# Performance work log

Measured on AMD Instinct MI355X. Metric: run time of the kernel, lower is better.

The kernel has to match this reference:

```python
import jax, jax.numpy as jnp
from jax import lax
import numpy as np

N_MTF = 41

def _gaussian2d(N, std):
    t = np.arange(-(N - 1) / 2, (N + 1) / 2)
    t1, t2 = np.meshgrid(t, t)
    return np.exp(-0.5 * (t1 / std) ** 2) * np.exp(-0.5 * (t2 / std) ** 2)

def _kaiser2d(N, beta):
    t = np.arange(-(N - 1) / 2, (N + 1) / 2) / np.double(N - 1)
    t1, t2 = np.meshgrid(t, t)
    t12 = np.sqrt(t1 * t1 + t2 * t2)
    w1 = np.kaiser(N, beta)
    w = np.interp(t12, t, w1)
    w[t12 > t[-1]] = 0
    w[t12 < t[0]] = 0
    return w

def _fir_filter_wind(Hd, w):
    hd = np.rot90(np.fft.fftshift(np.rot90(Hd, 2)), 2)
    h = np.fft.fftshift(np.fft.ifft2(hd))
    h = np.rot90(h, 2)
    return h * w

def gen_mtf_kernels(ratio, nbands):
    GNyq = np.asarray([0.34, 0.32, 0.3, 0.22], dtype='float32')[:nbands]  # QB sensor
    h = np.zeros((nbands, N_MTF, N_MTF), dtype='float32')
    fcut = 1.0 / ratio
    for ii in range(nbands):
        alpha = np.sqrt(((N_MTF - 1) * (fcut / 2)) ** 2 / (-2 * np.log(GNyq[ii])))
        H = _gaussian2d(N_MTF, alpha)
        Hd = H / np.max(H)
        w = _kaiser2d(N_MTF, 0.5)
        h[ii] = np.real(_fir_filter_wind(Hd, w)).astype('float32')
    return h

def gen_interp23_kernel():
    cdf23 = 2.0 * np.array([0.5, 0.305334091185, 0.0, -0.072698593239, 0.0,
                            0.021809577942, 0.0, -0.005192756653, 0.0,
                            0.000807762146, 0.0, -6.0081482e-05])
    d = cdf23[::-1]
    return np.concatenate([d[:-1], cdf23]).astype('float32')  # 23 taps

_DN = ('NCHW', 'OIHW', 'NCHW')

def _sep_filter_circular(img, k):
    # img: (bs, c, H, W); k: (K,) separable kernel, circular padding per torch F.pad('circular')
    bs, c, H, W = img.shape
    P = (k.shape[0] - 1) // 2
    f = img.reshape(bs * c, 1, H, W)
    f = jnp.pad(f, ((0, 0), (0, 0), (0, 0), (P, P)), mode='wrap')
    f = lax.conv_general_dilated(f, k.reshape(1, 1, 1, -1), (1, 1), 'VALID', dimension_numbers=_DN)
    f = jnp.pad(f, ((0, 0), (0, 0), (P, P), (0, 0)), mode='wrap')
    f = lax.conv_general_dilated(f, k.reshape(1, 1, -1, 1), (1, 1), 'VALID', dimension_numbers=_DN)
    return f.reshape(bs, c, H, W)

def interp23tap(x, kernel, num_upsamples):
    cur = x
    for k in range(num_upsamples):
        bs, c, h, w = cur.shape
        up = jnp.zeros((bs, c, 2 * h, 2 * w), cur.dtype)
        if k == 0:
            up = up.at[..., 1::2, 1::2].set(cur)
        else:
            up = up.at[..., ::2, ::2].set(cur)
        cur = _sep_filter_circular(up, kernel)
    return cur

def setup_inputs() -> dict:
    key = jax.random.key(0)
    bs, nbands, H, W = 4, 4, 1024, 1024
    ratio = 4
    x = jax.random.normal(key, (bs, nbands, H, W), dtype=jnp.float32)
    mtf_kernels = jnp.asarray(gen_mtf_kernels(ratio, nbands))          # (nbands, 41, 41)
    interp_kernel = jnp.asarray(gen_interp23_kernel())                  # (23,)
    pan_weights = jnp.full((nbands,), 1.0 / nbands, dtype=jnp.float32)  # 'mean' pan weights
    return {"x": x, "mtf_kernels": mtf_kernels, "interp_kernel": interp_kernel,
            "pan_weights": pan_weights, "ratio": ratio}

def reference(x, mtf_kernels, interp_kernel, pan_weights, ratio):
    # Simulated PAN: spectral weighting of HR bands
    pan = jnp.einsum('bchw,c->bhw', x, pan_weights)[:, None]  # (bs,1,H,W)
    # MTF blur: depthwise 41x41 conv with replicate padding
    nbands = x.shape[1]
    pad = mtf_kernels.shape[-1] // 2
    xp = jnp.pad(x, ((0, 0), (0, 0), (pad, pad), (pad, pad)), mode='edge')
    blurred = lax.conv_general_dilated(xp, mtf_kernels[:, None], (1, 1), 'VALID',
                                       dimension_numbers=_DN, feature_group_count=nbands)
    # Downsample: avgpool with kernel=stride=ratio
    bs, c, H, W = blurred.shape
    lrms = blurred.reshape(bs, c, H // ratio, ratio, W // ratio, ratio).mean(axis=(3, 5))
    # Upsample back via 23-tap polynomial interpolation (ratio = 2**num_upsamples)
    num_ups = int(ratio).bit_length() - 1
    ms_up = interp23tap(lrms, interp_kernel, num_ups)
    return pan, lrms, ms_up
```

## Files before the change

kernel.cpp:

```cpp
#include <hip/hip_runtime.h>

#define LRMS_OFF 4194304
#define MS_OFF  5242880

__global__ __launch_bounds__(256) void build_keff_kernel(
    const float* __restrict__ mtf, float* __restrict__ keff) {
  int e = blockIdx.x * 256 + threadIdx.x;
  if (e >= 4 * 44 * 44) return;
  int c = e / 1936;
  int rem = e - c * 1936;
  int p = rem / 44;
  int q = rem - p * 44;
  float s = 0.f;
  for (int di = 0; di < 4; ++di) {
    int u = p - di;
    if (u < 0 || u > 40) continue;
    for (int dj = 0; dj < 4; ++dj) {
      int v = q - dj;
      if (v < 0 || v > 40) continue;
      s += mtf[(c * 41 + u) * 41 + v];
    }
  }
  keff[e] = s * 0.0625f;
}

__global__ void build_gcoef_kernel(const float* __restrict__ ik,
                                   float* __restrict__ G) {
  int tid = threadIdx.x;
  if (tid >= 68) return;
  int d = tid / 17, oi = tid % 17, o = oi - 8;
  float k2[12];
  #pragma unroll
  for (int t = 0; t < 12; ++t) k2[t] = ik[2 * t];
  float g = 0.f;
  if (d == 0) {
    int t = o + 6;
    if (t >= 0 && t < 12) g = k2[t];
  } else if (d == 2) {
    g = (o == 0) ? 1.f : 0.f;
  } else if (d == 1) {
    int t = 2 * (o + 3);
    if (t >= 0 && t <= 10) g += k2[t];
    for (int t1 = 1; t1 < 12; t1 += 2) {
      int r = o + 6 - (t1 - 5) / 2;
      if (r >= 0 && r < 12) g += k2[t1] * k2[r];
    }
  } else {
    int t = 2 * o + 5;
    if (t >= 1 && t <= 11) g += k2[t];
    for (int t0 = 0; t0 <= 10; t0 += 2) {
      int r = o + 8 - t0 / 2;
      if (r >= 0 && r < 12) g += k2[t0] * k2[r];
    }
  }
  G[d * 17 + oi] = g;
}

__global__ __launch_bounds__(256) void pan_kernel(
    const float* __restrict__ x, const float* __restrict__ w,
    float* __restrict__ pan) {
  int g = blockIdx.x * 256 + threadIdx.x;
  int b = g >> 18;
  int e = g & 262143;
  const float4* x4 = (const float4*)x;
  float w0 = w[0], w1 = w[1], w2 = w[2], w3 = w[3];
  float4 a0 = x4[(size_t)(b * 4 + 0) * 262144 + e];
  float4 a1 = x4[(size_t)(b * 4 + 1) * 262144 + e];
  float4 a2 = x4[(size_t)(b * 4 + 2) * 262144 + e];
  float4 a3 = x4[(size_t)(b * 4 + 3) * 262144 + e];
  float4 o;
  o.x = a0.x * w0 + a1.x * w1 + a2.x * w2 + a3.x * w3;
  o.y = a0.y * w0 + a1.y * w1 + a2.y * w2 + a3.y * w3;
  o.z = a0.z * w0 + a1.z * w1 + a2.z * w2 + a3.z * w3;
  o.w = a0.w * w0 + a1.w * w1 + a2.w * w2 + a3.w * w3;
  ((float4*)pan)[g] = o;
}

__global__ __launch_bounds__(256) void lrms_kernel(
    const float* __restrict__ x, const float* __restrict__ keff,
    float* __restrict__ lrms) {
  int img = blockIdx.y;
  int ch  = img & 3;
  int i0  = blockIdx.x * 4;
  int oc  = threadIdx.x;

  const float* ximg = x + (size_t)img * 1048576;
  const float* Kc   = keff + ch * 1936;

  float4 acc[4];
  #pragma unroll
  for (int r = 0; r < 4; ++r) acc[r] = make_float4(0.f, 0.f, 0.f, 0.f);

  int c4base = oc - 5;
  bool interior = (oc >= 5) && (oc <= 250);
  float4 va[11], vb[11];

  auto loadrow = [&](int tt, float4* v) {
    int gy = 4 * i0 - 20 + tt;
    gy = gy < 0 ? 0 : (gy > 1023 ? 1023 : gy);
    const float4* row4 = (const float4*)(ximg + (size_t)gy * 1024);
    if (interior) {
      #pragma unroll
      for (int a = 0; a < 11; ++a) v[a] = row4[c4base + a];
    } else {
      const float* rowf = (const float*)row4;
      #pragma unroll
      for (int a = 0; a < 11; ++a) {
        int c4 = c4base + a;
        if ((unsigned)c4 <= 255u) {
          v[a] = row4[c4];
        } else {
          float4 t;
          t.x = rowf[min(max(4 * c4 + 0, 0), 1023)];
          t.y = rowf[min(max(4 * c4 + 1, 0), 1023)];
          t.z = rowf[min(max(4 * c4 + 2, 0), 1023)];
          t.w = rowf[min(max(4 * c4 + 3, 0), 1023)];
          v[a] = t;
        }
      }
    }
  };

  auto compute = [&](int tt, const float4* v) {
    #pragma unroll
    for (int r = 0; r < 4; ++r) {
      int p = tt - 4 * r;
      if ((unsigned)p < 44u) {
        const float* Kr = Kc + __builtin_amdgcn_readfirstlane(p * 44);
        float4 s = acc[r];
        #pragma unroll
        for (int a = 0; a < 11; ++a) {
          s.x += v[a].x * Kr[4 * a + 0];
          s.y += v[a].y * Kr[4 * a + 1];
          s.z += v[a].z * Kr[4 * a + 2];
          s.w += v[a].w * Kr[4 * a + 3];
        }
        acc[r] = s;
      }
    }
  };

  loadrow(0, va);
  for (int it = 0; it < 28; ++it) {
    int tt = 2 * it;
    loadrow(tt + 1, vb);
    compute(tt, va);
    if (tt + 2 < 56) loadrow(tt + 2, va);
    compute(tt + 1, vb);
  }

  #pragma unroll
  for (int r = 0; r < 4; ++r) {
    float s = acc[r].x + acc[r].y + acc[r].z + acc[r].w;
    lrms[((size_t)img * 256 + i0 + r) * 256 + oc] = s;
  }
}

__global__ __launch_bounds__(256) void interp_kernel(
    const float* __restrict__ lrms, const float* __restrict__ G,
    float* __restrict__ ms) {
  __shared__ float lr[32][48];
  __shared__ float H[32][68];
  __shared__ float Gs[4][17];

  int img = blockIdx.z;
  int bx = blockIdx.x, by = blockIdx.y;
  int tid = threadIdx.x;

  if (tid < 68) Gs[tid / 17][tid % 17] = G[tid];

  const float* L = lrms + (size_t)img * 65536;
  int ybase = by * 16 - 8, xbase = bx * 16 - 8;
  for (int e = tid; e < 1024; e += 256) {
    int yy = e >> 5, xx = e & 31;
    lr[yy][xx] = L[((ybase + yy) & 255) * 256 + ((xbase + xx) & 255)];
  }
  __syncthreads();

  for (int u = tid; u < 512; u += 256) {
    int r = u >> 4, j = u & 15;
    float t[17];
    #pragma unroll
    for (int o = 0; o < 17; ++o) t[o] = lr[r][j + o];
    float h0 = 0.f, h1 = 0.f, h3 = 0.f;
    #pragma unroll
    for (int o = 2; o <= 13; ++o) h0 += Gs[0][o] * t[o];
    #pragma unroll
    for (int o = 0; o < 17; ++o) h1 += Gs[1][o] * t[o];
    #pragma unroll
    for (int o = 0; o < 17; ++o) h3 += Gs[3][o] * t[o];
    float4 hv = make_float4(h0, h1, t[8], h3);
    *(float4*)(&H[r][4 * j]) = hv;
  }
  __syncthreads();

  float* O = ms + (size_t)img * 1048576 + (size_t)(by * 64) * 1024 + bx * 64;
  for (int u = tid; u < 1024; u += 256) {
    int il = u >> 6, X = u & 63;
    float t[17];
    #pragma unroll
    for (int o = 0; o < 17; ++o) t[o] = H[il + o][X];
    float v0 = 0.f, v1 = 0.f, v3 = 0.f;
    #pragma unroll
    for (int o = 2; o <= 13; ++o) v0 += Gs[0][o] * t[o];
    #pragma unroll
    for (int o = 0; o < 17; ++o) v1 += Gs[1][o] * t[o];
    #pragma unroll
    for (int o = 0; o < 17; ++o) v3 += Gs[3][o] * t[o];
    O[(size_t)(4 * il + 0) * 1024 + X] = v0;
    O[(size_t)(4 * il + 1) * 1024 + X] = v1;
    O[(size_t)(4 * il + 2) * 1024 + X] = t[8];
    O[(size_t)(4 * il + 3) * 1024 + X] = v3;
  }
}

extern "C" void kernel_launch(void* const* d_in, const int* in_sizes, int n_in,
                              void* d_out, int out_size, void* d_ws, size_t ws_size,
                              hipStream_t stream) {
  const float* x   = (const float*)d_in[0];
  const float* mtf = (const float*)d_in[1];
  const float* ik  = (const float*)d_in[2];
  const float* pw  = (const float*)d_in[3];
  float* out = (float*)d_out;
  float* keff = (float*)d_ws;
  float* G    = keff + 7744;

  build_keff_kernel<<<31, 256, 0, stream>>>(mtf, keff);
  build_gcoef_kernel<<<1, 128, 0, stream>>>(ik, G);
  pan_kernel<<<4096, 256, 0, stream>>>(x, pw, out);
  lrms_kernel<<<dim3(64, 16), 256, 0, stream>>>(x, keff, out + LRMS_OFF);
  interp_kernel<<<dim3(16, 16, 16), 256, 0, stream>>>(out + LRMS_OFF, G, out + MS_OFF);
}
```

Measured before the change: 330.2 us.

## Register-block lrms conv over four output columns per thread; merge coefficient kernels

The lrms blur+pool kernel now has each thread compute four adjacent output columns for four output rows. It loads a sliding window of 14 float4s per input row and reuses them across the four columns, so each loaded row serves 4x more outputs and global/cache traffic per output drops. Edge clamping is folded into a branch-free clamp-and-broadcast. Each wave now handles a 4-row band, the grid shrinks to 256 blocks, and launch bounds are set to one block per CU. That raises register pressure and leaves fewer waves to hide latency. The two tiny coefficient-setup kernels are merged into one launch to save launch overhead.

```diff
diff --git a/kernel.cpp b/kernel.cpp
--- a/kernel.cpp
+++ b/kernel.cpp
@@ -3,57 +3,57 @@
 #define LRMS_OFF 4194304
 #define MS_OFF  5242880
 
-__global__ __launch_bounds__(256) void build_keff_kernel(
-    const float* __restrict__ mtf, float* __restrict__ keff) {
-  int e = blockIdx.x * 256 + threadIdx.x;
-  if (e >= 4 * 44 * 44) return;
-  int c = e / 1936;
-  int rem = e - c * 1936;
-  int p = rem / 44;
-  int q = rem - p * 44;
-  float s = 0.f;
-  for (int di = 0; di < 4; ++di) {
-    int u = p - di;
-    if (u < 0 || u > 40) continue;
-    for (int dj = 0; dj < 4; ++dj) {
-      int v = q - dj;
-      if (v < 0 || v > 40) continue;
-      s += mtf[(c * 41 + u) * 41 + v];
-    }
-  }
-  keff[e] = s * 0.0625f;
-}
-
-__global__ void build_gcoef_kernel(const float* __restrict__ ik,
-                                   float* __restrict__ G) {
-  int tid = threadIdx.x;
-  if (tid >= 68) return;
-  int d = tid / 17, oi = tid % 17, o = oi - 8;
-  float k2[12];
-  #pragma unroll
-  for (int t = 0; t < 12; ++t) k2[t] = ik[2 * t];
-  float g = 0.f;
-  if (d == 0) {
-    int t = o + 6;
-    if (t >= 0 && t < 12) g = k2[t];
-  } else if (d == 2) {
-    g = (o == 0) ? 1.f : 0.f;
-  } else if (d == 1) {
-    int t = 2 * (o + 3);
-    if (t >= 0 && t <= 10) g += k2[t];
-    for (int t1 = 1; t1 < 12; t1 += 2) {
-      int r = o + 6 - (t1 - 5) / 2;
-      if (r >= 0 && r < 12) g += k2[t1] * k2[r];
-    }
+__global__ __launch_bounds__(256) void build_coefs_kernel(
+    const float* __restrict__ mtf, const float* __restrict__ ik,
+    float* __restrict__ keff, float* __restrict__ G) {
+  if (blockIdx.x < 31) {
+    int e = blockIdx.x * 256 + threadIdx.x;
+    if (e >= 4 * 44 * 44) return;
+    int c = e / 1936;
+    int rem = e - c * 1936;
+    int p = rem / 44;
+    int q = rem - p * 44;
+    float s = 0.f;
+    for (int di = 0; di < 4; ++di) {
+      int u = p - di;
+      if (u < 0 || u > 40) continue;
+      for (int dj = 0; dj < 4; ++dj) {
+        int v = q - dj;
+        if (v < 0 || v > 40) continue;
+        s += mtf[(c * 41 + u) * 41 + v];
+      }
+    }
+    keff[e] = s * 0.0625f;
   } else {
-    int t = 2 * o + 5;
-    if (t >= 1 && t <= 11) g += k2[t];
-    for (int t0 = 0; t0 <= 10; t0 += 2) {
-      int r = o + 8 - t0 / 2;
-      if (r >= 0 && r < 12) g += k2[t0] * k2[r];
-    }
-  }
-  G[d * 17 + oi] = g;
+    int tid = threadIdx.x;
+    if (tid >= 68) return;
+    int d = tid / 17, oi = tid % 17, o = oi - 8;
+    float k2[12];
+    #pragma unroll
+    for (int t = 0; t < 12; ++t) k2[t] = ik[2 * t];
+    float g = 0.f;
+    if (d == 0) {
+      int t = o + 6;
+      if (t >= 0 && t < 12) g = k2[t];
+    } else if (d == 2) {
+      g = (o == 0) ? 1.f : 0.f;
+    } else if (d == 1) {
+      int t = 2 * (o + 3);
+      if (t >= 0 && t <= 10) g += k2[t];
+      for (int t1 = 1; t1 < 12; t1 += 2) {
+        int r = o + 6 - (t1 - 5) / 2;
+        if (r >= 0 && r < 12) g += k2[t1] * k2[r];
+      }
+    } else {
+      int t = 2 * o + 5;
+      if (t >= 1 && t <= 11) g += k2[t];
+      for (int t0 = 0; t0 <= 10; t0 += 2) {
+        int r = o + 8 - t0 / 2;
+        if (r >= 0 && r < 12) g += k2[t0] * k2[r];
+      }
+    }
+    G[d * 17 + oi] = g;
+  }
 }
 
 __global__ __launch_bounds__(256) void pan_kernel(
@@ -76,83 +76,78 @@
   ((float4*)pan)[g] = o;
 }
 
-__global__ __launch_bounds__(256) void lrms_kernel(
+__global__ __launch_bounds__(256, 1) void lrms_kernel(
     const float* __restrict__ x, const float* __restrict__ keff,
     float* __restrict__ lrms) {
   int img = blockIdx.y;
   int ch  = img & 3;
-  int i0  = blockIdx.x * 4;
-  int oc  = threadIdx.x;
+  int w   = threadIdx.x >> 6;
+  int lane = threadIdx.x & 63;
+  int I0  = blockIdx.x * 16 + w * 4;
 
   const float* ximg = x + (size_t)img * 1048576;
   const float* Kc   = keff + ch * 1936;
 
-  float4 acc[4];
+  float acc[4][4];
   #pragma unroll
-  for (int r = 0; r < 4; ++r) acc[r] = make_float4(0.f, 0.f, 0.f, 0.f);
-
-  int c4base = oc - 5;
-  bool interior = (oc >= 5) && (oc <= 250);
-  float4 va[11], vb[11];
-
-  auto loadrow = [&](int tt, float4* v) {
-    int gy = 4 * i0 - 20 + tt;
+  for (int r = 0; r < 4; ++r)
+    #pragma unroll
+    for (int c = 0; c < 4; ++c) acc[r][c] = 0.f;
+
+  int c4base = 4 * lane - 5;
+  float4 Wa[14], Wb[14];
+
+  auto loadrow = [&](int tt, float4* W) {
+    int gy = 4 * I0 - 20 + tt;
     gy = gy < 0 ? 0 : (gy > 1023 ? 1023 : gy);
     const float4* row4 = (const float4*)(ximg + (size_t)gy * 1024);
-    if (interior) {
-      #pragma unroll
-      for (int a = 0; a < 11; ++a) v[a] = row4[c4base + a];
-    } else {
-      const float* rowf = (const float*)row4;
-      #pragma unroll
-      for (int a = 0; a < 11; ++a) {
-        int c4 = c4base + a;
-        if ((unsigned)c4 <= 255u) {
-          v[a] = row4[c4];
-        } else {
-          float4 t;
-          t.x = rowf[min(max(4 * c4 + 0, 0), 1023)];
-          t.y = rowf[min(max(4 * c4 + 1, 0), 1023)];
-          t.z = rowf[min(max(4 * c4 + 2, 0), 1023)];
-          t.w = rowf[min(max(4 * c4 + 3, 0), 1023)];
-          v[a] = t;
-        }
-      }
+    #pragma unroll
+    for (int j = 0; j < 14; ++j) {
+      int idx = c4base + j;
+      int ic = idx < 0 ? 0 : (idx > 255 ? 255 : idx);
+      float4 t = row4[ic];
+      if (j <= 4) {
+        if (idx < 0) t = make_float4(t.x, t.x, t.x, t.x);
+      }
+      if (j >= 9) {
+        if (idx > 255) t = make_float4(t.w, t.w, t.w, t.w);
+      }
+      W[j] = t;
     }
   };
 
-  auto compute = [&](int tt, const float4* v) {
+  auto compute = [&](int tt, const float4* W) {
     #pragma unroll
     for (int r = 0; r < 4; ++r) {
       int p = tt - 4 * r;
       if ((unsigned)p < 44u) {
         const float* Kr = Kc + __builtin_amdgcn_readfirstlane(p * 44);
-        float4 s = acc[r];
         #pragma unroll
         for (int a = 0; a < 11; ++a) {
-          s.x += v[a].x * Kr[4 * a + 0];
-          s.y += v[a].y * Kr[4 * a + 1];
-          s.z += v[a].z * Kr[4 * a + 2];
-          s.w += v[a].w * Kr[4 * a + 3];
+          float k0 = Kr[4 * a + 0], k1 = Kr[4 * a + 1];
+          float k2 = Kr[4 * a + 2], k3 = Kr[4 * a + 3];
+          #pragma unroll
+          for (int c = 0; c < 4; ++c) {
+            float4 v = W[c + a];
+            acc[r][c] += v.x * k0 + v.y * k1 + v.z * k2 + v.w * k3;
+          }
         }
-        acc[r] = s;
       }
     }
   };
 
-  loadrow(0, va);
-  for (int it = 0; it < 28; ++it) {
-    int tt = 2 * it;
-    loadrow(tt + 1, vb);
-    compute(tt, va);
-    if (tt + 2 < 56) loadrow(tt + 2, va);
-    compute(tt + 1, vb);
+  loadrow(0, Wa);
+  for (int tt = 0; tt < 56; tt += 2) {
+    loadrow(tt + 1, Wb);
+    compute(tt, Wa);
+    if (tt + 2 < 56) loadrow(tt + 2, Wa);
+    compute(tt + 1, Wb);
   }
 
   #pragma unroll
   for (int r = 0; r < 4; ++r) {
-    float s = acc[r].x + acc[r].y + acc[r].z + acc[r].w;
-    lrms[((size_t)img * 256 + i0 + r) * 256 + oc] = s;
+    float4 res = make_float4(acc[r][0], acc[r][1], acc[r][2], acc[r][3]);
+    ((float4*)lrms)[((size_t)img * 256 + I0 + r) * 64 + lane] = res;
   }
 }
 
@@ -189,8 +184,7 @@
     for (int o = 0; o < 17; ++o) h1 += Gs[1][o] * t[o];
     #pragma unroll
     for (int o = 0; o < 17; ++o) h3 += Gs[3][o] * t[o];
-    float4 hv = make_float4(h0, h1, t[8], h3);
-    *(float4*)(&H[r][4 * j]) = hv;
+    *(float4*)(&H[r][4 * j]) = make_float4(h0, h1, t[8], h3);
   }
   __syncthreads();
 
@@ -225,9 +219,8 @@
   float* keff = (float*)d_ws;
   float* G    = keff + 7744;
 
-  build_keff_kernel<<<31, 256, 0, stream>>>(mtf, keff);
-  build_gcoef_kernel<<<1, 128, 0, stream>>>(ik, G);
+  build_coefs_kernel<<<32, 256, 0, stream>>>(mtf, ik, keff, G);
   pan_kernel<<<4096, 256, 0, stream>>>(x, pw, out);
-  lrms_kernel<<<dim3(64, 16), 256, 0, stream>>>(x, keff, out + LRMS_OFF);
+  lrms_kernel<<<dim3(16, 16), 256, 0, stream>>>(x, keff, out + LRMS_OFF);
   interp_kernel<<<dim3(16, 16, 16), 256, 0, stream>>>(out + LRMS_OFF, G, out + MS_OFF);
 }
```

Measured after the change: 290.1 us. 12.1% less time.
